# Performance work log

Measured on AMD Instinct MI355X. Metric: run time of the kernel, lower is better.

## Reference

```python
import jax, jax.numpy as jnp
import numpy as np

FILL_VAL = -1
B, S, H, L = 16, 512, 768, 25


def _lstm_dir(x, w_ih, w_hh, b_ih, b_hh, reverse=False):
    # x: [B,T,I]; PyTorch gate order i,f,g,o
    if reverse:
        x = x[:, ::-1]
    xg = jnp.einsum('bti,gi->btg', x, w_ih) + b_ih + b_hh  # [B,T,4H]
    nh = w_hh.shape[1]

    def step(carry, xt):
        h, c = carry
        g = xt + h @ w_hh.T
        i, f, gg, o = jnp.split(g, 4, axis=-1)
        c = jax.nn.sigmoid(f) * c + jax.nn.sigmoid(i) * jnp.tanh(gg)
        h = jax.nn.sigmoid(o) * jnp.tanh(c)
        return (h, c), h

    z = jnp.zeros((x.shape[0], nh), x.dtype)
    _, hs = jax.lax.scan(step, (z, z), jnp.swapaxes(xg, 0, 1))
    hs = jnp.swapaxes(hs, 0, 1)  # [B,T,H]
    return hs[:, ::-1] if reverse else hs


def _crf_nll(emissions, tags, mask, trans, start, end):
    # torchcrf-style NLL, reduction='token_mean'. emissions [B,T,L], tags [B,T], mask bool [B,T]
    maskf = mask.astype(emissions.dtype)
    emit = jnp.take_along_axis(emissions, tags[..., None], axis=-1)[..., 0]  # [B,T]
    trans_sc = trans[tags[:, :-1], tags[:, 1:]]  # [B,T-1]
    num = start[tags[:, 0]] + emit[:, 0] + jnp.sum((trans_sc + emit[:, 1:]) * maskf[:, 1:], axis=1)
    lengths = mask.sum(axis=1)
    last_tags = tags[jnp.arange(tags.shape[0]), lengths - 1]
    num = num + end[last_tags]

    em_t = jnp.swapaxes(emissions, 0, 1)  # [T,B,L]
    mk_t = jnp.swapaxes(mask, 0, 1)

    def step(alpha, inp):
        e_t, m_t = inp
        nxt = jax.nn.logsumexp(alpha[:, :, None] + trans[None] + e_t[:, None, :], axis=1)
        return jnp.where(m_t[:, None], nxt, alpha), None

    alpha0 = start[None] + em_t[0]
    alpha, _ = jax.lax.scan(step, alpha0, (em_t[1:], mk_t[1:]))
    denom = jax.nn.logsumexp(alpha + end[None], axis=1)
    llh = num - denom
    return -(llh.sum() / maskf.sum())


def setup_inputs() -> dict:
    key = jax.random.key(0)
    ks = jax.random.split(key, 32)

    def u(k, shape, s):
        return jax.random.uniform(k, shape, jnp.float32, -s, s)

    s = 1.0 / float(np.sqrt(H))
    hidden = jax.random.normal(ks[0], (B, S, H), jnp.float32)
    labels = jax.random.randint(ks[1], (B, S), 0, L)
    lengths = jax.random.randint(ks[2], (B,), S // 2, S + 1)
    targets = jnp.where(jnp.arange(S)[None, :] < lengths[:, None], labels, FILL_VAL).astype(jnp.int32)

    inp = {'hidden': hidden, 'targets': targets}
    # 2-layer bidirectional LSTM params; layer 1 input is 2H
    names = [('l0', H), ('l0r', H), ('l1', 2 * H), ('l1r', 2 * H)]
    ki = 3
    for nm, insz in names:
        inp['w_ih_' + nm] = u(ks[ki], (4 * H, insz), s); ki += 1
        inp['w_hh_' + nm] = u(ks[ki], (4 * H, H), s); ki += 1
        inp['b_ih_' + nm] = u(ks[ki], (4 * H,), s); ki += 1
        inp['b_hh_' + nm] = u(ks[ki], (4 * H,), s); ki += 1
    inp['clf_w'] = u(ks[ki], (L, 2 * H), 1.0 / float(np.sqrt(2 * H))); ki += 1
    inp['clf_b'] = u(ks[ki], (L,), 1.0 / float(np.sqrt(2 * H))); ki += 1
    inp['crf_trans'] = u(ks[ki], (L, L), 0.1); ki += 1
    inp['crf_start'] = u(ks[ki], (L,), 0.1); ki += 1
    inp['crf_end'] = u(ks[ki], (L,), 0.1)
    return inp


def reference(hidden, targets,
              w_ih_l0, w_hh_l0, b_ih_l0, b_hh_l0,
              w_ih_l0r, w_hh_l0r, b_ih_l0r, b_hh_l0r,
              w_ih_l1, w_hh_l1, b_ih_l1, b_hh_l1,
              w_ih_l1r, w_hh_l1r, b_ih_l1r, b_hh_l1r,
              clf_w, clf_b, crf_trans, crf_start, crf_end):
    mask = targets != FILL_VAL
    tags = jnp.where(mask, targets, 0)
    h1 = jnp.concatenate([
        _lstm_dir(hidden, w_ih_l0, w_hh_l0, b_ih_l0, b_hh_l0),
        _lstm_dir(hidden, w_ih_l0r, w_hh_l0r, b_ih_l0r, b_hh_l0r, reverse=True)], axis=-1)
    h2 = jnp.concatenate([
        _lstm_dir(h1, w_ih_l1, w_hh_l1, b_ih_l1, b_hh_l1),
        _lstm_dir(h1, w_ih_l1r, w_hh_l1r, b_ih_l1r, b_hh_l1r, reverse=True)], axis=-1)
    logits = jnp.tanh(h2) @ clf_w.T + clf_b  # [B,S,L]
    return _crf_nll(logits, tags, mask, crf_trans, crf_start, crf_end)
```

## Files before the change

kernel.cpp:

```cpp
#include <hip/hip_runtime.h>
#include <cstdint>
#include <cstddef>

#define B   16
#define SEQ 512
#define HD  768
#define G4  3072
#define NL  25
#define NBLK 96

using u16 = unsigned short;
using u32 = uint32_t;
using u64 = unsigned long long;

__device__ __forceinline__ float bf2f(u16 u){
  union { float f; u32 i; } v; v.i = ((u32)u) << 16; return v.f;
}
__device__ __forceinline__ u16 f2bf(float f){
  union { float f; u32 i; } v; v.f = f;
  u32 r = v.i + 0x7FFFu + ((v.i >> 16) & 1u);
  return (u16)(r >> 16);
}
__device__ __forceinline__ float asf(u32 u){ union { float f; u32 i; } v; v.i = u; return v.f; }
__device__ __forceinline__ float sigm(float x){ return 1.f/(1.f + __expf(-x)); }
__device__ __forceinline__ float tanhfast(float x){ return 1.f - 2.f/(__expf(2.f*x) + 1.f); }

typedef __attribute__((ext_vector_type(8))) short bf16x8;
typedef __attribute__((ext_vector_type(4))) float f32x4;

__device__ __forceinline__ void stage_to_lds(u16* dst, const u16* src){
  *(uint4*)dst = *(const uint4*)src;
}
__device__ __forceinline__ void stage_to_lds(u16* dst, const float* src){
  float4 a = *(const float4*)src;
  float4 b = *(const float4*)(src + 4);
  uint4 v;
  v.x = (u32)f2bf(a.x) | ((u32)f2bf(a.y) << 16);
  v.y = (u32)f2bf(a.z) | ((u32)f2bf(a.w) << 16);
  v.z = (u32)f2bf(b.x) | ((u32)f2bf(b.y) << 16);
  v.w = (u32)f2bf(b.z) | ((u32)f2bf(b.w) << 16);
  *(uint4*)dst = v;
}

struct BPtrs { const float* bi[4]; const float* bh[4]; };

__global__ void prep_bias(BPtrs p, float* __restrict__ bias){
  int idx = blockIdx.x*blockDim.x + threadIdx.x;
  if (idx < 4*G4){
    int lid = idx / G4, g = idx % G4;
    bias[idx] = p.bi[lid][g] + p.bh[lid][g];
  }
}

template<typename AT>
__global__ __launch_bounds__(256) void gemm_xg_mfma(const AT* __restrict__ A, int K,
    const float* __restrict__ W, const float* __restrict__ bias, u16* __restrict__ out)
{
  __shared__ u16 As[128][40];
  __shared__ u16 Bs[128][40];
  const int tid = threadIdx.x;
  const int bm = blockIdx.y * 128;
  const int bn = blockIdx.x * 128;
  const int wid = tid >> 6, lane = tid & 63;
  const int wr = wid >> 1, wc = wid & 1;
  const int kq = lane >> 4, rl = lane & 15;

  f32x4 acc[4][4];
  #pragma unroll
  for (int mf = 0; mf < 4; mf++)
    #pragma unroll
    for (int nf = 0; nf < 4; nf++) acc[mf][nf] = (f32x4){0.f,0.f,0.f,0.f};

  for (int k0 = 0; k0 < K; k0 += 32){
    #pragma unroll
    for (int u = 0; u < 2; u++){
      int c = tid + u*256;
      int r = c >> 2, q = c & 3;
      stage_to_lds(&As[r][q*8], A + (size_t)(bm + r)*K + k0 + q*8);
      stage_to_lds(&Bs[r][q*8], W + (size_t)(bn + r)*K + k0 + q*8);
    }
    __syncthreads();
    bf16x8 af[4], bfr[4];
    #pragma unroll
    for (int mf = 0; mf < 4; mf++) af[mf]  = *(const bf16x8*)&As[wr*64 + mf*16 + rl][kq*8];
    #pragma unroll
    for (int nf = 0; nf < 4; nf++) bfr[nf] = *(const bf16x8*)&Bs[wc*64 + nf*16 + rl][kq*8];
    #pragma unroll
    for (int mf = 0; mf < 4; mf++)
      #pragma unroll
      for (int nf = 0; nf < 4; nf++)
        acc[mf][nf] = __builtin_amdgcn_mfma_f32_16x16x32_bf16(af[mf], bfr[nf], acc[mf][nf], 0, 0, 0);
    __syncthreads();
  }

  float bv[4];
  #pragma unroll
  for (int nf = 0; nf < 4; nf++) bv[nf] = bias[bn + wc*64 + nf*16 + rl];
  #pragma unroll
  for (int mf = 0; mf < 4; mf++){
    #pragma unroll
    for (int i = 0; i < 4; i++){
      size_t row = (size_t)bm + wr*64 + mf*16 + kq*4 + i;
      u16* op = out + row*G4 + bn + wc*64 + rl;
      #pragma unroll
      for (int nf = 0; nf < 4; nf++)
        op[nf*16] = f2bf(acc[mf][nf][i] + bv[nf]);
    }
  }
}

template<int LAYER>
__global__ __launch_bounds__(256, 1) void scan_kernel(
    const u16* __restrict__ xg,
    const float* __restrict__ whh_f,
    const float* __restrict__ whh_r,
    u16* __restrict__ hgbu,
    u32* __restrict__ flags,
    u16* __restrict__ hout)
{
  __shared__ float red[32*16*4];
  __shared__ float cL[128];

  const int tid  = threadIdx.x;
  const int dir  = blockIdx.x / NBLK;
  const int js   = blockIdx.x % NBLK;
  const int w    = tid >> 6;
  const int lane = tid & 63;
  const int lr   = lane & 15;
  const int lq   = lane >> 4;

  const float* Wsrc = dir ? whh_r : whh_f;

  bf16x8 af[2][6];
  #pragma unroll
  for (int m = 0; m < 2; m++){
    int j_local = m*16 + lr;
    int j_glob  = (j_local >> 3)*768 + js*8 + (j_local & 7);
    const float* rowp = Wsrc + (size_t)j_glob*HD;
    #pragma unroll
    for (int c = 0; c < 6; c++){
      int k = w*192 + c*32 + lq*8;
      float4 a  = *(const float4*)(rowp + k);
      float4 b4 = *(const float4*)(rowp + k + 4);
      union { u32 u[4]; bf16x8 v; } t;
      t.u[0] = (u32)f2bf(a.x)  | ((u32)f2bf(a.y)  << 16);
      t.u[1] = (u32)f2bf(a.z)  | ((u32)f2bf(a.w)  << 16);
      t.u[2] = (u32)f2bf(b4.x) | ((u32)f2bf(b4.y) << 16);
      t.u[3] = (u32)f2bf(b4.z) | ((u32)f2bf(b4.w) << 16);
      af[m][c] = t.v;
    }
  }
  if (tid < 128) cL[tid] = 0.f;
  __syncthreads();

  const int jh_l = tid >> 4;
  const int b_g  = tid & 15;
  u32* myflags = flags + dir*NBLK;

  for (int s = 0; s < SEQ; s++){
    const int t_seq = dir ? (SEQ-1-s) : s;

    float xgv[4];
    if (tid < 128){
      const u16* xp = xg + (((size_t)(dir*B + b_g))*SEQ + t_seq)*G4 + js*8 + jh_l;
      #pragma unroll
      for (int g = 0; g < 4; g++) xgv[g] = bf2f(xp[g*HD]);
    }

    if (s > 0){
      if (tid < NBLK){
        while (__hip_atomic_load(&myflags[tid], __ATOMIC_RELAXED, __HIP_MEMORY_SCOPE_AGENT) < (u32)s)
          __builtin_amdgcn_s_sleep(1);
      }
      __syncthreads();
    }

    const u16* hb = hgbu + (size_t)((s&1)*2 + dir)*(16*768) + lr*768;
    u64 bq[6][2];
    #pragma unroll
    for (int c = 0; c < 6; c++){
      const u64* p = (const u64*)(hb + w*192 + c*32 + lq*8);
      bq[c][0] = __hip_atomic_load(p,     __ATOMIC_RELAXED, __HIP_MEMORY_SCOPE_AGENT);
      bq[c][1] = __hip_atomic_load(p + 1, __ATOMIC_RELAXED, __HIP_MEMORY_SCOPE_AGENT);
    }

    f32x4 acc0 = (f32x4){0.f,0.f,0.f,0.f};
    f32x4 acc1 = (f32x4){0.f,0.f,0.f,0.f};
    #pragma unroll
    for (int c = 0; c < 6; c++){
      union { u64 q[2]; bf16x8 v; } bu;
      bu.q[0] = bq[c][0]; bu.q[1] = bq[c][1];
      acc0 = __builtin_amdgcn_mfma_f32_16x16x32_bf16(af[0][c], bu.v, acc0, 0, 0, 0);
      acc1 = __builtin_amdgcn_mfma_f32_16x16x32_bf16(af[1][c], bu.v, acc1, 0, 0, 0);
    }

    #pragma unroll
    for (int i = 0; i < 4; i++){
      red[(( 0 + lq*4 + i)*16 + lr)*4 + w] = acc0[i];
      red[((16 + lq*4 + i)*16 + lr)*4 + w] = acc1[i];
    }
    __syncthreads();

    const bool more = (s + 1 < SEQ);
    u32 opair = 0;
    if (tid < 128){
      float gs[4];
      #pragma unroll
      for (int g = 0; g < 4; g++){
        const float4 r4 = *(const float4*)&red[((g*8 + jh_l)*16 + b_g)*4];
        gs[g] = r4.x + r4.y + r4.z + r4.w + xgv[g];
      }
      float c  = cL[tid];
      float ct = sigm(gs[1])*c + sigm(gs[0])*tanhfast(gs[2]);
      float h  = sigm(gs[3])*tanhfast(ct);
      cL[tid] = ct;

      u32 hb16 = (u32)f2bf(h);
      u32 hoth = (u32)__shfl_xor((int)hb16, 16);
      float hw = (LAYER == 0) ? h : tanhfast(h);
      u32 ob16 = (u32)f2bf(hw);
      u32 ooth = (u32)__shfl_xor((int)ob16, 16);
      opair = (ob16 & 0xffffu) | (ooth << 16);

      if (more && (tid & 16) == 0){
        u32 pair = (hb16 & 0xffffu) | (hoth << 16);
        u16* hdst = hgbu + (size_t)(((s+1)&1)*2 + dir)*(16*768) + b_g*768 + js*8 + jh_l;
        __hip_atomic_store((u32*)hdst, pair, __ATOMIC_RELAXED, __HIP_MEMORY_SCOPE_AGENT);
      }
    }
    if (more){
      __syncthreads();
      if (tid == 0)
        __hip_atomic_store(&myflags[js], (u32)(s+1), __ATOMIC_RELAXED, __HIP_MEMORY_SCOPE_AGENT);
    }
    if (tid < 128 && (tid & 16) == 0){
      u16* od = hout + ((size_t)b_g*SEQ + t_seq)*1536 + dir*HD + js*8 + jh_l;
      *(u32*)od = opair;
    }
  }
}

__global__ __launch_bounds__(256) void logits_kernel(const u16* __restrict__ th,
    const float* __restrict__ clf_w, const float* __restrict__ clf_b,
    float* __restrict__ logits)
{
  __shared__ u16 xl[8*1536];
  const int tid = threadIdx.x;
  const int row0 = blockIdx.x * 8;
  {
    const uint4* src = (const uint4*)(th + (size_t)row0*1536);
    uint4* dst = (uint4*)xl;
    #pragma unroll
    for (int i = 0; i < 6; i++) dst[i*256 + tid] = src[i*256 + tid];
  }
  __syncthreads();
  const int r = tid >> 5, l = tid & 31;
  if (l < NL){
    float acc = clf_b[l];
    const float* wr = clf_w + (size_t)l*1536;
    #pragma unroll 2
    for (int kk = 0; kk < 192; kk++){
      uint4 xv = *(const uint4*)&xl[r*1536 + kk*8];
      float4 w0 = *(const float4*)(wr + kk*8);
      float4 w1 = *(const float4*)(wr + kk*8 + 4);
      acc = fmaf(asf(xv.x<<16), w0.x, acc); acc = fmaf(asf(xv.x&0xffff0000u), w0.y, acc);
      acc = fmaf(asf(xv.y<<16), w0.z, acc); acc = fmaf(asf(xv.y&0xffff0000u), w0.w, acc);
      acc = fmaf(asf(xv.z<<16), w1.x, acc); acc = fmaf(asf(xv.z&0xffff0000u), w1.y, acc);
      acc = fmaf(asf(xv.w<<16), w1.z, acc); acc = fmaf(asf(xv.w&0xffff0000u), w1.w, acc);
    }
    logits[(size_t)(row0 + r)*NL + l] = acc;
  }
}

__global__ __launch_bounds__(256) void crf_num(const float* __restrict__ logits,
    const int* __restrict__ targets, const float* __restrict__ trans,
    const float* __restrict__ start, const float* __restrict__ endv,
    float* __restrict__ numlen)
{
  const int b = blockIdx.x;
  const int* tg = targets + (size_t)b*SEQ;
  float s = 0.f; int cnt = 0;
  for (int t = threadIdx.x; t < SEQ; t += 256){
    int cur = tg[t];
    if (cur >= 0){
      cnt++;
      float e = logits[((size_t)b*SEQ + t)*NL + cur];
      s += e;
      if (t > 0) s += trans[tg[t-1]*NL + cur];
    }
  }
  __shared__ float ss[256]; __shared__ int sc[256];
  ss[threadIdx.x] = s; sc[threadIdx.x] = cnt;
  __syncthreads();
  for (int o = 128; o > 0; o >>= 1){
    if (threadIdx.x < o){ ss[threadIdx.x] += ss[threadIdx.x+o]; sc[threadIdx.x] += sc[threadIdx.x+o]; }
    __syncthreads();
  }
  if (threadIdx.x == 0){
    int len = sc[0];
    numlen[b]      = ss[0] + start[tg[0]] + endv[tg[len-1]];
    numlen[16 + b] = (float)len;
  }
}

__global__ __launch_bounds__(64) void crf_fwd(const float* __restrict__ logits,
    const int* __restrict__ targets, const float* __restrict__ trans,
    const float* __restrict__ start, const float* __restrict__ endv,
    float* __restrict__ denom)
{
  const int b = blockIdx.x, lane = threadIdx.x;
  __shared__ float tr[NL*NL];
  for (int i = lane; i < NL*NL; i += 64) tr[i] = trans[i];
  __syncthreads();
  const bool act = lane < NL;
  const int j = act ? lane : 0;
  float alpha = act ? (start[j] + logits[(size_t)b*SEQ*NL + j]) : -3e38f;
  const int* tg = targets + (size_t)b*SEQ;
  for (int t = 1; t < SEQ; t++){
    if (tg[t] < 0) break;
    float e = logits[((size_t)b*SEQ + t)*NL + j];
    float v[NL]; float mx = -3e38f;
    #pragma unroll
    for (int i = 0; i < NL; i++){
      float ai = __shfl(alpha, i);
      v[i] = ai + tr[i*NL + j];
      mx = fmaxf(mx, v[i]);
    }
    float sum = 0.f;
    #pragma unroll
    for (int i = 0; i < NL; i++) sum += __expf(v[i] - mx);
    float nxt = mx + __logf(sum) + e;
    if (act) alpha = nxt;
  }
  float x = act ? alpha + endv[j] : -3e38f;
  float m2 = x;
  #pragma unroll
  for (int off = 32; off >= 1; off >>= 1) m2 = fmaxf(m2, __shfl_xor(m2, off));
  float se = __expf(x - m2);
  #pragma unroll
  for (int off = 32; off >= 1; off >>= 1) se += __shfl_xor(se, off);
  if (lane == 0) denom[b] = m2 + __logf(se);
}

__global__ void crf_final(const float* __restrict__ numlen, const float* __restrict__ denom,
                          float* __restrict__ out)
{
  if (blockIdx.x == 0 && threadIdx.x == 0){
    float sn = 0.f, sl = 0.f;
    for (int b = 0; b < 16; b++){ sn += numlen[b] - denom[b]; sl += numlen[16+b]; }
    out[0] = -sn / sl;
  }
}

extern "C" void kernel_launch(void* const* d_in, const int* in_sizes, int n_in,
                              void* d_out, int out_size, void* d_ws, size_t ws_size,
                              hipStream_t stream)
{
  const float* hidden  = (const float*)d_in[0];
  const int*   targets = (const int*)  d_in[1];
  const float* w_ih[4] = {(const float*)d_in[2], (const float*)d_in[6], (const float*)d_in[10], (const float*)d_in[14]};
  const float* w_hh[4] = {(const float*)d_in[3], (const float*)d_in[7], (const float*)d_in[11], (const float*)d_in[15]};
  const float* b_ih[4] = {(const float*)d_in[4], (const float*)d_in[8], (const float*)d_in[12], (const float*)d_in[16]};
  const float* b_hh[4] = {(const float*)d_in[5], (const float*)d_in[9], (const float*)d_in[13], (const float*)d_in[17]};
  const float* clf_w = (const float*)d_in[18];
  const float* clf_b = (const float*)d_in[19];
  const float* trans = (const float*)d_in[20];
  const float* start = (const float*)d_in[21];
  const float* endv  = (const float*)d_in[22];

  char* p = (char*)d_ws;
  auto alloc = [&](size_t bytes){ void* r = (void*)p; p += (bytes + 255) & ~(size_t)255; return r; };
  float* bias   = (float*)alloc((size_t)4*G4*4);
  u16*   xg     = (u16*)  alloc((size_t)2*B*SEQ*G4*2);
  u16*   h1     = (u16*)  alloc((size_t)B*SEQ*2*HD*2);
  u16*   hgbu   = (u16*)  alloc((size_t)2*2*16*768*2);
  u32*   flags  = (u32*)  alloc((size_t)2*NBLK*4);
  float* logits = (float*)alloc((size_t)B*SEQ*NL*4);
  float* numlen = (float*)alloc(32*4);
  float* denom  = (float*)alloc(16*4);
  if ((size_t)(p - (char*)d_ws) > ws_size) return;

  BPtrs bp;
  for (int i = 0; i < 4; i++){ bp.bi[i] = b_ih[i]; bp.bh[i] = b_hh[i]; }
  prep_bias<<<48, 256, 0, stream>>>(bp, bias);

  const dim3 ggrid(24, 64);
  const size_t xg_dir = (size_t)B*SEQ*G4;
  const size_t hgb_bytes = (size_t)2*2*16*768*2;
  const size_t flg_bytes = (size_t)2*NBLK*4;

  gemm_xg_mfma<float><<<ggrid, 256, 0, stream>>>(hidden, HD, w_ih[0], bias + 0*G4, xg);
  gemm_xg_mfma<float><<<ggrid, 256, 0, stream>>>(hidden, HD, w_ih[1], bias + 1*G4, xg + xg_dir);
  hipMemsetAsync(hgbu, 0, hgb_bytes, stream);
  hipMemsetAsync(flags, 0, flg_bytes, stream);
  {
    const u16* a0 = xg; const float* a1 = w_hh[0]; const float* a2 = w_hh[1];
    u16* a3 = hgbu; u32* a4 = flags; u16* a5 = h1;
    void* args[] = { &a0, &a1, &a2, &a3, &a4, &a5 };
    hipLaunchCooperativeKernel(reinterpret_cast<void*>(&scan_kernel<0>),
                               dim3(192), dim3(256), args, 0, stream);
  }

  gemm_xg_mfma<u16><<<ggrid, 256, 0, stream>>>(h1, 2*HD, w_ih[2], bias + 2*G4, xg);
  gemm_xg_mfma<u16><<<ggrid, 256, 0, stream>>>(h1, 2*HD, w_ih[3], bias + 3*G4, xg + xg_dir);
  hipMemsetAsync(hgbu, 0, hgb_bytes, stream);
  hipMemsetAsync(flags, 0, flg_bytes, stream);
  {
    const u16* a0 = xg; const float* a1 = w_hh[2]; const float* a2 = w_hh[3];
    u16* a3 = hgbu; u32* a4 = flags; u16* a5 = h1;
    void* args[] = { &a0, &a1, &a2, &a3, &a4, &a5 };
    hipLaunchCooperativeKernel(reinterpret_cast<void*>(&scan_kernel<1>),
                               dim3(192), dim3(256), args, 0, stream);
  }

  logits_kernel<<<1024, 256, 0, stream>>>(h1, clf_w, clf_b, logits);
  crf_num<<<16, 256, 0, stream>>>(logits, targets, trans, start, endv, numlen);
  crf_fwd<<<16, 64, 0, stream>>>(logits, targets, trans, start, endv, denom);
  crf_final<<<1, 64, 0, stream>>>(numlen, denom, (float*)d_out);
}
```

Measured before the change: 4.083 ms.

## Relayout xg and h exchange buffers, use per-wave flags, stage CRF logits in LDS

The input-gate GEMM now writes xg in a block-major layout, so each scan block reads one contiguous 128-element chunk per timestep instead of strided rows. The h exchange buffer is laid out per block so that loads are contiguous. The block-wide flag barrier (poll by thread, then __syncthreads) is replaced with per-wave flag polling using __all, and each wave publishes its own flag after s_waitcnt. This is meant to cut the latency of each sequential step. The CRF forward kernel also copies each batch's logits into LDS before its loop. The trade-offs are an extra __syncthreads in the scan step and relaxed-ordering memory semantics that rely on vmcnt waits.

New measurement: 5.615 ms. +37.5%, slower.

```diff
diff --git a/kernel.cpp b/kernel.cpp
--- a/kernel.cpp
+++ b/kernel.cpp
@@ -12,6 +12,8 @@
 using u16 = unsigned short;
 using u32 = uint32_t;
 using u64 = unsigned long long;
+
+#define XGD ((size_t)NBLK*SEQ*512)
 
 __device__ __forceinline__ float bf2f(u16 u){
   union { float f; u32 i; } v; v.i = ((u32)u) << 16; return v.f;
@@ -94,24 +96,31 @@
   }
 
   float bv[4];
-  #pragma unroll
-  for (int nf = 0; nf < 4; nf++) bv[nf] = bias[bn + wc*64 + nf*16 + rl];
+  size_t coloff[4];
+  #pragma unroll
+  for (int nf = 0; nf < 4; nf++){
+    int n = bn + wc*64 + nf*16 + rl;
+    bv[nf] = bias[n];
+    int g = n / 768, j = n - g*768;
+    coloff[nf] = (size_t)(j >> 3)*262144 + (size_t)g*128 + (j & 7);
+  }
   #pragma unroll
   for (int mf = 0; mf < 4; mf++){
     #pragma unroll
     for (int i = 0; i < 4; i++){
-      size_t row = (size_t)bm + wr*64 + mf*16 + kq*4 + i;
-      u16* op = out + row*G4 + bn + wc*64 + rl;
+      int row = bm + wr*64 + mf*16 + kq*4 + i;
+      int b = row >> 9, t = row & 511;
+      size_t rowoff = (size_t)t*512 + (size_t)b*8;
       #pragma unroll
       for (int nf = 0; nf < 4; nf++)
-        op[nf*16] = f2bf(acc[mf][nf][i] + bv[nf]);
+        out[coloff[nf] + rowoff] = f2bf(acc[mf][nf][i] + bv[nf]);
     }
   }
 }
 
 template<int LAYER>
 __global__ __launch_bounds__(256, 1) void scan_kernel(
-    const u16* __restrict__ xg,
+    const u16* __restrict__ xgp,
     const float* __restrict__ whh_f,
     const float* __restrict__ whh_r,
     u16* __restrict__ hgbu,
@@ -155,33 +164,36 @@
 
   const int jh_l = tid >> 4;
   const int b_g  = tid & 15;
-  u32* myflags = flags + dir*NBLK;
+  const u32* myflags = flags + dir*192 + w*48;
+  u32* setflag = flags + dir*192 + js*2;
+  const bool needf = lane < 48;
+  const u32* fp = myflags + (needf ? lane : 0);
 
   for (int s = 0; s < SEQ; s++){
     const int t_seq = dir ? (SEQ-1-s) : s;
 
     float xgv[4];
     if (tid < 128){
-      const u16* xp = xg + (((size_t)(dir*B + b_g))*SEQ + t_seq)*G4 + js*8 + jh_l;
+      const u16* xp = xgp + (size_t)dir*XGD + (size_t)js*262144
+                    + (size_t)t_seq*512 + b_g*8 + jh_l;
       #pragma unroll
-      for (int g = 0; g < 4; g++) xgv[g] = bf2f(xp[g*HD]);
-    }
-
-    if (s > 0){
-      if (tid < NBLK){
-        while (__hip_atomic_load(&myflags[tid], __ATOMIC_RELAXED, __HIP_MEMORY_SCOPE_AGENT) < (u32)s)
-          __builtin_amdgcn_s_sleep(1);
-      }
-      __syncthreads();
-    }
-
-    const u16* hb = hgbu + (size_t)((s&1)*2 + dir)*(16*768) + lr*768;
+      for (int g = 0; g < 4; g++) xgv[g] = bf2f(xp[g*128]);
+    }
+
+    while (true){
+      u32 v = __hip_atomic_load(fp, __ATOMIC_RELAXED, __HIP_MEMORY_SCOPE_AGENT);
+      if (__all(!needf || v >= (u32)s)) break;
+    }
+
+    const u16* hbase = hgbu + (size_t)((s&1)*2 + dir)*12288;
     u64 bq[6][2];
     #pragma unroll
     for (int c = 0; c < 6; c++){
-      const u64* p = (const u64*)(hb + w*192 + c*32 + lq*8);
-      bq[c][0] = __hip_atomic_load(p,     __ATOMIC_RELAXED, __HIP_MEMORY_SCOPE_AGENT);
-      bq[c][1] = __hip_atomic_load(p + 1, __ATOMIC_RELAXED, __HIP_MEMORY_SCOPE_AGENT);
+      int jsc = w*24 + c*4 + lq;
+      bq[c][0] = __hip_atomic_load((const u64*)(hbase + jsc*128 + lr*4),
+                                   __ATOMIC_RELAXED, __HIP_MEMORY_SCOPE_AGENT);
+      bq[c][1] = __hip_atomic_load((const u64*)(hbase + jsc*128 + 64 + lr*4),
+                                   __ATOMIC_RELAXED, __HIP_MEMORY_SCOPE_AGENT);
     }
 
     f32x4 acc0 = (f32x4){0.f,0.f,0.f,0.f};
@@ -201,41 +213,47 @@
     }
     __syncthreads();
 
-    const bool more = (s + 1 < SEQ);
-    u32 opair = 0;
+    float gs[4];
     if (tid < 128){
-      float gs[4];
       #pragma unroll
       for (int g = 0; g < 4; g++){
         const float4 r4 = *(const float4*)&red[((g*8 + jh_l)*16 + b_g)*4];
         gs[g] = r4.x + r4.y + r4.z + r4.w + xgv[g];
       }
+    }
+    __syncthreads();
+
+    if (tid < 128){
       float c  = cL[tid];
       float ct = sigm(gs[1])*c + sigm(gs[0])*tanhfast(gs[2]);
       float h  = sigm(gs[3])*tanhfast(ct);
       cL[tid] = ct;
 
+      const bool more = (s + 1 < SEQ);
       u32 hb16 = (u32)f2bf(h);
       u32 hoth = (u32)__shfl_xor((int)hb16, 16);
       float hw = (LAYER == 0) ? h : tanhfast(h);
       u32 ob16 = (u32)f2bf(hw);
       u32 ooth = (u32)__shfl_xor((int)ob16, 16);
-      opair = (ob16 & 0xffffu) | (ooth << 16);
-
-      if (more && (tid & 16) == 0){
+
+      if (more && (jh_l & 1) == 0){
         u32 pair = (hb16 & 0xffffu) | (hoth << 16);
-        u16* hdst = hgbu + (size_t)(((s+1)&1)*2 + dir)*(16*768) + b_g*768 + js*8 + jh_l;
+        int half = jh_l >> 2;
+        u16* hdst = hgbu + (size_t)(((s+1)&1)*2 + dir)*12288
+                  + js*128 + half*64 + b_g*4 + (jh_l & 2);
         __hip_atomic_store((u32*)hdst, pair, __ATOMIC_RELAXED, __HIP_MEMORY_SCOPE_AGENT);
       }
-    }
-    if (more){
-      __syncthreads();
-      if (tid == 0)
-        __hip_atomic_store(&myflags[js], (u32)(s+1), __ATOMIC_RELAXED, __HIP_MEMORY_SCOPE_AGENT);
-    }
-    if (tid < 128 && (tid & 16) == 0){
-      u16* od = hout + ((size_t)b_g*SEQ + t_seq)*1536 + dir*HD + js*8 + jh_l;
-      *(u32*)od = opair;
+      if (more){
+        asm volatile("s_waitcnt vmcnt(0)" ::: "memory");
+        if ((tid & 63) == 0)
+          __hip_atomic_store(setflag + (tid >> 6), (u32)(s+1),
+                             __ATOMIC_RELAXED, __HIP_MEMORY_SCOPE_AGENT);
+      }
+      if ((jh_l & 1) == 0){
+        u32 opair = (ob16 & 0xffffu) | (ooth << 16);
+        u16* od = hout + ((size_t)b_g*SEQ + t_seq)*1536 + dir*HD + js*8 + jh_l;
+        *(u32*)od = opair;
+      }
     }
   }
 }
@@ -309,16 +327,22 @@
     float* __restrict__ denom)
 {
   const int b = blockIdx.x, lane = threadIdx.x;
+  __shared__ float el[SEQ*NL];
   __shared__ float tr[NL*NL];
   for (int i = lane; i < NL*NL; i += 64) tr[i] = trans[i];
+  {
+    const float4* src = (const float4*)(logits + (size_t)b*SEQ*NL);
+    float4* dst = (float4*)el;
+    for (int i = lane; i < SEQ*NL/4; i += 64) dst[i] = src[i];
+  }
   __syncthreads();
   const bool act = lane < NL;
   const int j = act ? lane : 0;
-  float alpha = act ? (start[j] + logits[(size_t)b*SEQ*NL + j]) : -3e38f;
+  float alpha = act ? (start[j] + el[j]) : -3e38f;
   const int* tg = targets + (size_t)b*SEQ;
   for (int t = 1; t < SEQ; t++){
     if (tg[t] < 0) break;
-    float e = logits[((size_t)b*SEQ + t)*NL + j];
+    float e = el[t*NL + j];
     float v[NL]; float mx = -3e38f;
     #pragma unroll
     for (int i = 0; i < NL; i++){
@@ -371,10 +395,10 @@
   char* p = (char*)d_ws;
   auto alloc = [&](size_t bytes){ void* r = (void*)p; p += (bytes + 255) & ~(size_t)255; return r; };
   float* bias   = (float*)alloc((size_t)4*G4*4);
-  u16*   xg     = (u16*)  alloc((size_t)2*B*SEQ*G4*2);
+  u16*   xgp    = (u16*)  alloc((size_t)2*XGD*2);
   u16*   h1     = (u16*)  alloc((size_t)B*SEQ*2*HD*2);
-  u16*   hgbu   = (u16*)  alloc((size_t)2*2*16*768*2);
-  u32*   flags  = (u32*)  alloc((size_t)2*NBLK*4);
+  u16*   hgbu   = (u16*)  alloc((size_t)2*2*12288*2);
+  u32*   flags  = (u32*)  alloc((size_t)2*192*4);
   float* logits = (float*)alloc((size_t)B*SEQ*NL*4);
   float* numlen = (float*)alloc(32*4);
   float* denom  = (float*)alloc(16*4);
@@ -385,28 +409,27 @@
   prep_bias<<<48, 256, 0, stream>>>(bp, bias);
 
   const dim3 ggrid(24, 64);
-  const size_t xg_dir = (size_t)B*SEQ*G4;
-  const size_t hgb_bytes = (size_t)2*2*16*768*2;
-  const size_t flg_bytes = (size_t)2*NBLK*4;
-
-  gemm_xg_mfma<float><<<ggrid, 256, 0, stream>>>(hidden, HD, w_ih[0], bias + 0*G4, xg);
-  gemm_xg_mfma<float><<<ggrid, 256, 0, stream>>>(hidden, HD, w_ih[1], bias + 1*G4, xg + xg_dir);
+  const size_t hgb_bytes = (size_t)2*2*12288*2;
+  const size_t flg_bytes = (size_t)2*192*4;
+
+  gemm_xg_mfma<float><<<ggrid, 256, 0, stream>>>(hidden, HD, w_ih[0], bias + 0*G4, xgp);
+  gemm_xg_mfma<float><<<ggrid, 256, 0, stream>>>(hidden, HD, w_ih[1], bias + 1*G4, xgp + XGD);
   hipMemsetAsync(hgbu, 0, hgb_bytes, stream);
   hipMemsetAsync(flags, 0, flg_bytes, stream);
   {
-    const u16* a0 = xg; const float* a1 = w_hh[0]; const float* a2 = w_hh[1];
+    const u16* a0 = xgp; const float* a1 = w_hh[0]; const float* a2 = w_hh[1];
     u16* a3 = hgbu; u32* a4 = flags; u16* a5 = h1;
     void* args[] = { &a0, &a1, &a2, &a3, &a4, &a5 };
     hipLaunchCooperativeKernel(reinterpret_cast<void*>(&scan_kernel<0>),
                                dim3(192), dim3(256), args, 0, stream);
   }
 
-  gemm_xg_mfma<u16><<<ggrid, 256, 0, stream>>>(h1, 2*HD, w_ih[2], bias + 2*G4, xg);
-  gemm_xg_mfma<u16><<<ggrid, 256, 0, stream>>>(h1, 2*HD, w_ih[3], bias + 3*G4, xg + xg_dir);
+  gemm_xg_mfma<u16><<<ggrid, 256, 0, stream>>>(h1, 2*HD, w_ih[2], bias + 2*G4, xgp);
+  gemm_xg_mfma<u16><<<ggrid, 256, 0, stream>>>(h1, 2*HD, w_ih[3], bias + 3*G4, xgp + XGD);
   hipMemsetAsync(hgbu, 0, hgb_bytes, stream);
   hipMemsetAsync(flags, 0, flg_bytes, stream);
   {
-    const u16* a0 = xg; const float* a1 = w_hh[2]; const float* a2 = w_hh[3];
+    const u16* a0 = xgp; const float* a1 = w_hh[2]; const float* a2 = w_hh[3];
     u16* a3 = hgbu; u32* a4 = flags; u16* a5 = h1;
     void* args[] = { &a0, &a1, &a2, &a3, &a4, &a5 };
     hipLaunchCooperativeKernel(reinterpret_cast<void*>(&scan_kernel<1>),
```
